# Kernel tuning notes

Hardware: AMD Instinct MI355X
Metric: run time of the kernel (lower is better)

Reference implementation:

```python
import jax, jax.numpy as jnp
import numpy as np

TEMPERATURE = 8.0  # sqrt(head_dim=64)

def setup_inputs() -> dict:
    key = jax.random.key(0)
    kq, kk, kv, km = jax.random.split(key, 4)
    B, H, S, D = 2, 16, 2048, 64
    q = jax.random.normal(kq, (B, H, S, D), dtype=jnp.float32)
    k = jax.random.normal(kk, (B, H, S, D), dtype=jnp.float32)
    v = jax.random.normal(kv, (B, H, S, D), dtype=jnp.float32)
    mask = jax.random.randint(km, (B, 1, 1, S), 0, 2, dtype=jnp.int32)
    return {"q": q, "k": k, "v": v, "mask": mask}

def reference(q, k, v, mask):
    # attn = softmax((q/T) @ k^T) with mask fill of -1e9 (dropout p=0 -> no-op)
    attn = jnp.einsum("bhsd,bhtd->bhst", q / TEMPERATURE, k)  # [B,H,S,S]
    attn = jnp.where(mask == 0, jnp.float32(-1e9), attn)
    attn = jax.nn.softmax(attn, axis=-1)
    # output = v^T @ attn @ v  -> [B,H,D,D]
    out = jnp.einsum("bhsd,bhst->bhdt", v, attn)   # v.transpose(2,3) @ attn
    out = jnp.einsum("bhdt,bhtc->bhdc", out, v)     # @ v
    return (out, attn)
```

## Files before the change

kernel.cpp:

```cpp
#include <hip/hip_runtime.h>
#include <math.h>

#define S_LEN 2048
#define D_DIM 64
#define NBH   32
#define TINV  0.125f
#define C2    0.18033688011112042f

typedef float  f32x4   __attribute__((ext_vector_type(4)));
typedef float  f32x16  __attribute__((ext_vector_type(16)));
typedef short  s16x4   __attribute__((ext_vector_type(4)));
typedef short  s16x8   __attribute__((ext_vector_type(8)));
typedef unsigned u32x4 __attribute__((ext_vector_type(4)));
typedef __bf16 bf16x8  __attribute__((ext_vector_type(8)));

__device__ __forceinline__ short bfc(float f) {
  return __builtin_bit_cast(short, (__bf16)f);
}
__device__ __forceinline__ unsigned pk2(float lo, float hi) {
  unsigned r;
  asm("v_cvt_pk_bf16_f32 %0, %1, %2" : "=v"(r) : "v"(lo), "v"(hi));
  return r;
}

__device__ __forceinline__ f32x4 mfma16(s16x8 a, s16x8 b, f32x4 c) {
  return __builtin_amdgcn_mfma_f32_16x16x32_bf16(
      __builtin_bit_cast(bf16x8, a), __builtin_bit_cast(bf16x8, b), c, 0, 0, 0);
}
__device__ __forceinline__ f32x16 mfma32(s16x8 a, s16x8 b, f32x16 c) {
  return __builtin_amdgcn_mfma_f32_32x32x16_bf16(
      __builtin_bit_cast(bf16x8, a), __builtin_bit_cast(bf16x8, b), c, 0, 0, 0);
}

__device__ __forceinline__ short* ldsp(short* base, int row, int byteoff) {
  return (short*)((char*)base + row * 128 + (byteoff ^ ((row & 7) << 4)));
}

__global__ __launch_bounds__(256) void prep(
    const float* __restrict__ k, const float* __restrict__ v,
    short* __restrict__ kb16, short* __restrict__ vT)
{
  const int bid = blockIdx.x;
  const int t   = bid & 1023;
  const int bh  = t >> 5;
  const int kt  = t & 31;
  const int tid = threadIdx.x;

  if (bid < 1024) {
    const int st  = tid >> 2;
    const int sd0 = (tid & 3) * 16;
    const float* kp = k + ((size_t)bh * S_LEN + kt * 64 + st) * D_DIM + sd0;
    s16x8 o0, o1;
    #pragma unroll
    for (int j = 0; j < 8; ++j) { o0[j] = bfc(kp[j]); o1[j] = bfc(kp[8 + j]); }
    short* dst = kb16 + ((size_t)bh * S_LEN + kt * 64 + st) * D_DIM + sd0;
    *(s16x8*)dst       = o0;
    *(s16x8*)(dst + 8) = o1;
  } else {
    const int vt0 = (tid & 15) * 4;
    const int vd0 = (tid >> 4) * 4;
    const float* vb = v + ((size_t)bh * S_LEN + kt * 64) * D_DIM;
    f32x4 vr[4];
    #pragma unroll
    for (int i = 0; i < 4; ++i)
      vr[i] = *(const f32x4*)(vb + (size_t)(vt0 + i) * D_DIM + vd0);
    #pragma unroll
    for (int j = 0; j < 4; ++j) {
      s16x4 pk;
      pk[0] = bfc(vr[0][j]); pk[1] = bfc(vr[1][j]);
      pk[2] = bfc(vr[2][j]); pk[3] = bfc(vr[3][j]);
      *(s16x4*)(vT + (size_t)(bh * 64 + vd0 + j) * S_LEN + kt * 64 + vt0) = pk;
    }
  }
}

__global__ __launch_bounds__(256, 3) void attn_fwd(
    const float* __restrict__ q, const short* __restrict__ kb16,
    const short* __restrict__ vT, const int* __restrict__ mask,
    float* __restrict__ attn_out, short* __restrict__ OT)
{
  __shared__ short KV[2][64][64];
  __shared__ float rspart[4][32];

  short* KlB = &KV[0][0][0];
  short* VlB = &KV[1][0][0];

  const int bid   = blockIdx.x;
  const int xcd   = bid & 7;
  const int chunk = bid >> 3;
  const int bh    = xcd * 4 + (chunk >> 5);
  const int qt    = chunk & 31;
  const int b     = bh >> 4;

  const int tid  = threadIdx.x;
  const int wave = tid >> 6;
  const int lane = tid & 63;
  const int lr   = lane & 15;
  const int lg   = lane >> 4;
  const int L31  = lane & 31;
  const int hi   = lane >> 5;
  const int Q0   = qt * 64;

  const int qtile = wave & 1;
  const int tt    = wave >> 1;

  const short* kbb  = kb16 + (size_t)bh * S_LEN * D_DIM;
  const short* vtb  = vT   + (size_t)bh * 64 * S_LEN;
  const int*   mrow = mask + b * S_LEN;

  s16x8 aqv[4];
  {
    const float* qp = q + ((size_t)bh * S_LEN + Q0 + qtile * 32 + L31) * D_DIM + hi * 8;
    #pragma unroll
    for (int ks = 0; ks < 4; ++ks) {
      f32x4 x0 = *(const f32x4*)(qp + ks * 16);
      f32x4 x1 = *(const f32x4*)(qp + ks * 16 + 4);
      s16x8 f;
      #pragma unroll
      for (int j = 0; j < 4; ++j) { f[j] = bfc(x0[j]); f[4 + j] = bfc(x1[j]); }
      aqv[ks] = f;
    }
  }

  f32x16 oacc[2];
  #pragma unroll
  for (int dt = 0; dt < 2; ++dt)
    #pragma unroll
    for (int r = 0; r < 16; ++r) oacc[dt][r] = 0.f;
  float rs = 0.f;

  const int st = tid >> 2;
  const int c0 = (tid & 3) * 32;

  s16x8 kr0, kr1, vr0, vr1;
  kr0 = *(const s16x8*)(kbb + (size_t)st * D_DIM + c0 / 2);
  kr1 = *(const s16x8*)(kbb + (size_t)st * D_DIM + c0 / 2 + 8);
  vr0 = *(const s16x8*)(vtb + (size_t)st * S_LEN + c0 / 2);
  vr1 = *(const s16x8*)(vtb + (size_t)st * S_LEN + c0 / 2 + 8);

  for (int kt = 0; kt < 32; ++kt) {
    __syncthreads();
    *(s16x8*)ldsp(KlB, st, c0)      = kr0;
    *(s16x8*)ldsp(KlB, st, c0 + 16) = kr1;
    *(s16x8*)ldsp(VlB, st, c0)      = vr0;
    *(s16x8*)ldsp(VlB, st, c0 + 16) = vr1;
    __syncthreads();

    if (kt + 1 < 32) {
      kr0 = *(const s16x8*)(kbb + (size_t)((kt + 1) * 64 + st) * D_DIM + c0 / 2);
      kr1 = *(const s16x8*)(kbb + (size_t)((kt + 1) * 64 + st) * D_DIM + c0 / 2 + 8);
      vr0 = *(const s16x8*)(vtb + (size_t)st * S_LEN + (kt + 1) * 64 + c0 / 2);
      vr1 = *(const s16x8*)(vtb + (size_t)st * S_LEN + (kt + 1) * 64 + c0 / 2 + 8);
    }
    const unsigned long long mbits = __ballot(mrow[kt * 64 + lane] != 0);

    f32x16 sacc;
    #pragma unroll
    for (int r = 0; r < 16; ++r) sacc[r] = 0.f;
    #pragma unroll
    for (int ks = 0; ks < 4; ++ks) {
      s16x8 ak = *(const s16x8*)ldsp(KlB, tt * 32 + L31, ks * 32 + hi * 16);
      sacc = mfma32(ak, aqv[ks], sacc);
    }

    const unsigned mloc = (unsigned)(mbits >> (tt * 32 + hi * 4));
    #pragma unroll
    for (int r = 0; r < 16; ++r) {
      float e = __builtin_amdgcn_exp2f(sacc[r] * C2);
      e = ((mloc >> ((r & 3) + 8 * (r >> 2))) & 1u) ? e : 0.f;
      rs += e;
      sacc[r] = e;
    }

    unsigned a0 = pk2(sacc[0], sacc[1]),   b0 = pk2(sacc[4], sacc[5]);
    unsigned a1 = pk2(sacc[2], sacc[3]),   b1 = pk2(sacc[6], sacc[7]);
    unsigned a2 = pk2(sacc[8], sacc[9]),   b2 = pk2(sacc[12], sacc[13]);
    unsigned a3 = pk2(sacc[10], sacc[11]), b3 = pk2(sacc[14], sacc[15]);
    asm volatile("v_permlane32_swap_b32 %0, %1" : "+v"(a0), "+v"(b0));
    asm volatile("v_permlane32_swap_b32 %0, %1" : "+v"(a1), "+v"(b1));
    asm volatile("v_permlane32_swap_b32 %0, %1" : "+v"(a2), "+v"(b2));
    asm volatile("v_permlane32_swap_b32 %0, %1" : "+v"(a3), "+v"(b3));
    const s16x8 pb0 = __builtin_bit_cast(s16x8, (u32x4){a0, a1, b0, b1});
    const s16x8 pb1 = __builtin_bit_cast(s16x8, (u32x4){a2, a3, b2, b3});

    #pragma unroll
    for (int dt = 0; dt < 2; ++dt) {
      s16x8 bv0 = *(const s16x8*)ldsp(VlB, dt * 32 + L31, tt * 64 + hi * 16);
      s16x8 bv1 = *(const s16x8*)ldsp(VlB, dt * 32 + L31, tt * 64 + 32 + hi * 16);
      oacc[dt] = mfma32(bv0, pb0, oacc[dt]);
      oacc[dt] = mfma32(bv1, pb1, oacc[dt]);
    }
  }

  rs += __shfl_xor(rs, 32, 64);

  __syncthreads();
  if (lane < 32) rspart[wave][lane] = rs;
  float* oex = (float*)&KV[0][0][0];
  if (wave >= 2) {
    #pragma unroll
    for (int dt = 0; dt < 2; ++dt)
      #pragma unroll
      for (int r = 0; r < 16; ++r)
        oex[(wave - 2) * 2048 + dt * 1024 + r * 64 + lane] = oacc[dt][r];
  }
  __syncthreads();

  if (wave < 2) {
    const float rsum = rspart[wave][L31] + rspart[wave + 2][L31];
    const float rinvq = 1.0f / rsum;
    #pragma unroll
    for (int dt = 0; dt < 2; ++dt)
      #pragma unroll
      for (int r = 0; r < 16; ++r) {
        const int d = dt * 32 + (r & 3) + 8 * (r >> 2) + 4 * hi;
        float val = (oacc[dt][r] + oex[wave * 2048 + dt * 1024 + r * 64 + lane]) * rinvq;
        OT[(size_t)(bh * 64 + d) * S_LEN + Q0 + wave * 32 + L31] = bfc(val);
      }
  }

  const int qin = (wave & 1) * 16 + lr;
  const float l2r = -__log2f(rspart[wave >> 1][qin] + rspart[(wave >> 1) + 2][qin]);

  __syncthreads();

  s16x8 aq[2];
  {
    const float* qp = q + ((size_t)bh * S_LEN + Q0 + wave * 16 + lr) * D_DIM + lg * 8;
    #pragma unroll
    for (int kk = 0; kk < 2; ++kk) {
      f32x4 x0 = *(const f32x4*)(qp + kk * 32);
      f32x4 x1 = *(const f32x4*)(qp + kk * 32 + 4);
      s16x8 f;
      #pragma unroll
      for (int j = 0; j < 4; ++j) { f[j] = bfc(x0[j]); f[4 + j] = bfc(x1[j]); }
      aq[kk] = f;
    }
  }

  char* stb = (char*)&KV[0][0][0] + wave * 4096;
  float* abase = attn_out + (size_t)bh * S_LEN * S_LEN + (size_t)(Q0 + wave * 16) * S_LEN;
  const int rrow = lane >> 4;
  const int rcol = lane & 15;

  for (int kt = 0; kt < 32; ++kt) {
    const unsigned long long mbits = __ballot(mrow[kt * 64 + lane] != 0);

    #pragma unroll
    for (int n = 0; n < 4; ++n) {
      f32x4 sacc = (f32x4){0.f, 0.f, 0.f, 0.f};
      #pragma unroll
      for (int kk = 0; kk < 2; ++kk) {
        s16x8 bk = *(const s16x8*)(kbb + (size_t)(kt * 64 + n * 16 + lr) * D_DIM +
                                   kk * 32 + lg * 8);
        sacc = mfma16(bk, aq[kk], sacc);
      }
      const unsigned nib = (unsigned)(mbits >> (n * 16 + lg * 4)) & 0xFu;
      f32x4 pv;
      #pragma unroll
      for (int reg = 0; reg < 4; ++reg) {
        float e = __builtin_amdgcn_exp2f(fmaf(sacc[reg], C2, l2r));
        pv[reg] = (nib & (1u << reg)) ? e : 0.f;
      }
      *(f32x4*)(stb + lr * 256 + ((n * 64 + lg * 16) ^ ((lr & 7) << 4))) = pv;
    }

    #pragma unroll
    for (int i = 0; i < 4; ++i) {
      const int row = i * 4 + rrow;
      f32x4 val = *(const f32x4*)(stb + row * 256 + ((rcol * 16) ^ ((row & 7) << 4)));
      __builtin_nontemporal_store(val,
          (f32x4*)(abase + (size_t)row * S_LEN + kt * 64 + rcol * 4));
    }
  }
}

__global__ __launch_bounds__(256) void vo_gemm(
    const short* __restrict__ vT, const short* __restrict__ OT,
    float* __restrict__ out)
{
  const int bh   = blockIdx.x;
  const int tid  = threadIdx.x;
  const int wave = tid >> 6;
  const int lane = tid & 63;
  const int lr   = lane & 15;
  const int lg   = lane >> 4;

  const short* vb = vT + (size_t)(bh * 64) * S_LEN;
  const short* ob = OT + (size_t)(bh * 64) * S_LEN;

  f32x4 acc[4];
  #pragma unroll
  for (int n = 0; n < 4; ++n) acc[n] = (f32x4){0.f, 0.f, 0.f, 0.f};

  for (int s = 0; s < S_LEN; s += 32) {
    s16x8 a = *(const s16x8*)&vb[(size_t)(wave * 16 + lr) * S_LEN + s + lg * 8];
    #pragma unroll
    for (int n = 0; n < 4; ++n) {
      s16x8 bo = *(const s16x8*)&ob[(size_t)(n * 16 + lr) * S_LEN + s + lg * 8];
      acc[n] = mfma16(a, bo, acc[n]);
    }
  }

  #pragma unroll
  for (int n = 0; n < 4; ++n) {
    #pragma unroll
    for (int reg = 0; reg < 4; ++reg) {
      const int d = wave * 16 + lg * 4 + reg;
      const int c = n * 16 + lr;
      out[(size_t)(bh * 64 + d) * 64 + c] = acc[n][reg];
    }
  }
}

extern "C" void kernel_launch(void* const* d_in, const int* in_sizes, int n_in,
                              void* d_out, int out_size, void* d_ws, size_t ws_size,
                              hipStream_t stream) {
  (void)in_sizes; (void)n_in; (void)out_size; (void)ws_size;
  const float* q    = (const float*)d_in[0];
  const float* k    = (const float*)d_in[1];
  const float* v    = (const float*)d_in[2];
  const int*   mask = (const int*)d_in[3];

  float* out  = (float*)d_out;
  float* attn = out + (size_t)NBH * 64 * 64;

  const size_t HS = (size_t)NBH * 64 * S_LEN;
  short* OT   = (short*)d_ws;
  short* vT   = OT + HS;
  short* kb16 = vT + HS;

  prep<<<dim3(2048), dim3(256), 0, stream>>>(k, v, kb16, vT);
  attn_fwd<<<dim3(1024), dim3(256), 0, stream>>>(q, kb16, vT, mask, attn, OT);
  vo_gemm<<<dim3(NBH), dim3(256), 0, stream>>>(vT, OT, out);
}
```

Before: 221.6 us.

## Split fused attention kernel into row-sum/output pass and probability write pass

Measured after the change: 240.3 us. +8.4%, slower.

```diff
diff --git a/kernel.cpp b/kernel.cpp
--- a/kernel.cpp
+++ b/kernel.cpp
@@ -74,10 +74,10 @@
   }
 }
 
-__global__ __launch_bounds__(256, 3) void attn_fwd(
+__global__ __launch_bounds__(256, 4) void attn_o(
     const float* __restrict__ q, const short* __restrict__ kb16,
     const short* __restrict__ vT, const int* __restrict__ mask,
-    float* __restrict__ attn_out, short* __restrict__ OT)
+    short* __restrict__ OT, float* __restrict__ l2rs)
 {
   __shared__ short KV[2][64][64];
   __shared__ float rspart[4][32];
@@ -95,8 +95,6 @@
   const int tid  = threadIdx.x;
   const int wave = tid >> 6;
   const int lane = tid & 63;
-  const int lr   = lane & 15;
-  const int lg   = lane >> 4;
   const int L31  = lane & 31;
   const int hi   = lane >> 5;
   const int Q0   = qt * 64;
@@ -209,6 +207,8 @@
   if (wave < 2) {
     const float rsum = rspart[wave][L31] + rspart[wave + 2][L31];
     const float rinvq = 1.0f / rsum;
+    if (hi == 0)
+      l2rs[(size_t)bh * S_LEN + Q0 + wave * 32 + L31] = -__log2f(rsum);
     #pragma unroll
     for (int dt = 0; dt < 2; ++dt)
       #pragma unroll
@@ -218,11 +218,31 @@
         OT[(size_t)(bh * 64 + d) * S_LEN + Q0 + wave * 32 + L31] = bfc(val);
       }
   }
-
-  const int qin = (wave & 1) * 16 + lr;
-  const float l2r = -__log2f(rspart[wave >> 1][qin] + rspart[(wave >> 1) + 2][qin]);
-
-  __syncthreads();
+}
+
+__global__ __launch_bounds__(256, 4) void attn_p(
+    const float* __restrict__ q, const short* __restrict__ kb16,
+    const int* __restrict__ mask, const float* __restrict__ l2rs,
+    float* __restrict__ attn_out)
+{
+  __shared__ char stb_all[16384];
+
+  const int bid   = blockIdx.x;
+  const int xcd   = bid & 7;
+  const int chunk = bid >> 3;
+  const int bh    = xcd * 4 + (chunk >> 5);
+  const int qt    = chunk & 31;
+  const int b     = bh >> 4;
+
+  const int tid  = threadIdx.x;
+  const int wave = tid >> 6;
+  const int lane = tid & 63;
+  const int lr   = lane & 15;
+  const int lg   = lane >> 4;
+  const int Q0   = qt * 64;
+
+  const short* kbb  = kb16 + (size_t)bh * S_LEN * D_DIM;
+  const int*   mrow = mask + b * S_LEN;
 
   s16x8 aq[2];
   {
@@ -238,7 +258,9 @@
     }
   }
 
-  char* stb = (char*)&KV[0][0][0] + wave * 4096;
+  const float l2r = l2rs[(size_t)bh * S_LEN + Q0 + wave * 16 + lr];
+
+  char* stb = stb_all + wave * 4096;
   float* abase = attn_out + (size_t)bh * S_LEN * S_LEN + (size_t)(Q0 + wave * 16) * S_LEN;
   const int rrow = lane >> 4;
   const int rcol = lane & 15;
@@ -329,8 +351,10 @@
   short* OT   = (short*)d_ws;
   short* vT   = OT + HS;
   short* kb16 = vT + HS;
+  float* l2rs = (float*)(kb16 + HS);
 
   prep<<<dim3(2048), dim3(256), 0, stream>>>(k, v, kb16, vT);
-  attn_fwd<<<dim3(1024), dim3(256), 0, stream>>>(q, kb16, vT, mask, attn, OT);
+  attn_o<<<dim3(1024), dim3(256), 0, stream>>>(q, kb16, vT, mask, OT, l2rs);
+  attn_p<<<dim3(1024), dim3(256), 0, stream>>>(q, kb16, mask, l2rs, attn);
   vo_gemm<<<dim3(NBH), dim3(256), 0, stream>>>(vT, OT, out);
 }
```
